# Optimization experiments

Measured on AMD Instinct MI355X. Metric: run time of the kernel, lower is better.

## Reference

```python
import jax, jax.numpy as jnp
import numpy as np

B, L, D = 4096, 200, 128  # batch, neighbor bonds per molecule, bond feature dim
LN_EPS = 1e-5


def setup_inputs() -> dict:
    key = jax.random.key(0)
    ks = jax.random.split(key, 6)
    s = 1.0 / np.sqrt(D).astype(np.float32)
    return {
        "mol_bond_feature": jax.random.normal(ks[0], (B, D), jnp.float32),
        "bond_feature": jax.random.normal(ks[1], (B, L, D), jnp.float32),
        "mol_bond_attend_mask": jnp.ones((B, L, 1), jnp.float32),
        "mol_bond_softmax_mask": jnp.zeros((B, L, 1), jnp.float32),
        "W_self": jax.random.normal(ks[2], (D, D), jnp.float32) * s,   # mol_bond_fc
        "b_self": jnp.zeros((D,), jnp.float32),
        "W_nb": jax.random.normal(ks[3], (D, D), jnp.float32) * s,     # mol_bond_neighbor_fc
        "b_nb": jnp.zeros((D,), jnp.float32),
        "w_align": jax.random.normal(ks[4], (2 * D,), jnp.float32) * s,  # GAT align weight [2D]->1
        "b_align": jnp.zeros((), jnp.float32),
        "ln_gamma": jnp.ones((D,), jnp.float32),
        "ln_beta": jnp.zeros((D,), jnp.float32),
    }


def reference(mol_bond_feature, bond_feature, mol_bond_attend_mask,
              mol_bond_softmax_mask, W_self, b_self, W_nb, b_nb,
              w_align, b_align, ln_gamma, ln_beta):
    # Linear projections (dropout p=0 -> identity)
    x = mol_bond_feature @ W_self.T + b_self            # [B, D]
    y = jnp.einsum('bld,ed->ble', bond_feature, W_nb) + b_nb  # [B, L, D]

    # GAT align: Linear over concat([x_expand, y]) == split dot products (no concat materialized)
    wx, wy = w_align[:D], w_align[D:]
    score = (x @ wx)[:, None, None] + jnp.einsum('bld,d->bl', y, wy)[..., None] + b_align  # [B, L, 1]
    score = jax.nn.leaky_relu(score)                    # GNN_attn_act
    score = score + mol_bond_softmax_mask

    attn = jax.nn.softmax(score, axis=-2) * mol_bond_attend_mask  # [B, L, 1]
    ctx = jnp.sum(attn * y, axis=-2)                    # [B, D]

    # LayerNorm
    mu = jnp.mean(ctx, axis=-1, keepdims=True)
    var = jnp.mean(jnp.square(ctx - mu), axis=-1, keepdims=True)
    return (ctx - mu) * jax.lax.rsqrt(var + LN_EPS) * ln_gamma + ln_beta
```

## Files before the change

### kernel.cpp

```cpp
#include <hip/hip_runtime.h>
#include <math.h>

#define B_ 4096
#define L_ 200
#define D_ 128

typedef float f4 __attribute__((ext_vector_type(4)));

#define WS_AFIN 512
#define WS_WT   5120
#define WS_NEED ((size_t)(WS_WT + D_ * D_) * sizeof(float))

__global__ void prep_kernel(const float* __restrict__ W_self,
                            const float* __restrict__ W_nb,
                            const float* __restrict__ b_self,
                            const float* __restrict__ b_nb,
                            const float* __restrict__ w_align,
                            const float* __restrict__ b_align,
                            float* __restrict__ ws, int do_wt) {
  const int blk = blockIdx.x;
  const int t = threadIdx.x;
  if (blk == 0) {
    float su = 0.f, sv = 0.f;
    for (int e = 0; e < D_; ++e) {
      su = fmaf(w_align[e],      W_self[e * D_ + t], su);
      sv = fmaf(w_align[D_ + e], W_nb[e * D_ + t],   sv);
    }
    ws[t]      = su;
    ws[D_ + t] = sv;
    if (t == 0) {
      float cb = 0.f, cc = 0.f;
      for (int e = 0; e < D_; ++e) {
        cb = fmaf(b_self[e], w_align[e],      cb);
        cc = fmaf(b_nb[e],   w_align[D_ + e], cc);
      }
      ws[2 * D_]     = cb;
      ws[2 * D_ + 1] = cc + b_align[0];
    }
  } else if (do_wt) {
    const int d = blk - 1;
    ws[WS_WT + d * D_ + t] = W_nb[t * D_ + d];
  }
}

template <bool SPLIT>
__global__ __launch_bounds__(256) void mol_bond_stream(
    const float* __restrict__ mbf,
    const float* __restrict__ bond,
    const float* __restrict__ amask,
    const float* __restrict__ smask,
    const float* __restrict__ W_nb,
    const float* __restrict__ b_nb,
    const float* __restrict__ gamma,
    const float* __restrict__ beta,
    float* __restrict__ ws,
    float* __restrict__ out) {
  const int b    = blockIdx.x;
  const int tid  = threadIdx.x;
  const int w    = tid >> 6;
  const int lane = tid & 63;
  const int g    = lane >> 4;
  const int sl   = lane & 15;
  const int dA   = 4 * sl;
  const int dB   = 64 + 4 * sl;
  const int rg   = w * 4 + g;

  __shared__ float am_s[L_];
  __shared__ float sm_s[L_];
  __shared__ float g_l[16][D_];
  __shared__ float sA[16][2];
  __shared__ float gfin[D_];
  __shared__ float ctx_l[D_];
  __shared__ float Afin_s;

  for (int l0 = tid; l0 < L_; l0 += 256) {
    am_s[l0] = amask[(size_t)b * L_ + l0];
    sm_s[l0] = smask[(size_t)b * L_ + l0];
  }

  const f4 uA = *(const f4*)(ws + dA);
  const f4 uB = *(const f4*)(ws + dB);
  const f4 vA = *(const f4*)(ws + D_ + dA);
  const f4 vB = *(const f4*)(ws + D_ + dB);
  const float cb = ws[2 * D_], cc = ws[2 * D_ + 1];

  const f4 mA = *(const f4*)(mbf + (size_t)b * D_ + dA);
  const f4 mB = *(const f4*)(mbf + (size_t)b * D_ + dB);
  float xp = mA.x * uA.x + mA.y * uA.y + mA.z * uA.z + mA.w * uA.w
           + mB.x * uB.x + mB.y * uB.y + mB.z * uB.z + mB.w * uB.w;
  xp += __shfl_xor(xp, 8, 64);
  xp += __shfl_xor(xp, 4, 64);
  xp += __shfl_xor(xp, 2, 64);
  xp += __shfl_xor(xp, 1, 64);
  const float xc = xp + cb + cc;

  __syncthreads();

  float s = 0.f, A = 0.f;
  f4 gA = {0.f, 0.f, 0.f, 0.f};
  f4 gB = {0.f, 0.f, 0.f, 0.f};
  const float* bb = bond + (size_t)b * (L_ * D_);

  auto body = [&](int l) {
    f4 fA = __builtin_nontemporal_load((const f4*)(bb + l * D_ + dA));
    f4 fB = __builtin_nontemporal_load((const f4*)(bb + l * D_ + dB));
    float t = fA.x * vA.x + fA.y * vA.y + fA.z * vA.z + fA.w * vA.w
            + fB.x * vB.x + fB.y * vB.y + fB.z * vB.z + fB.w * vB.w;
    t += __shfl_xor(t, 8, 64);
    t += __shfl_xor(t, 4, 64);
    t += __shfl_xor(t, 2, 64);
    t += __shfl_xor(t, 1, 64);
    float sc = xc + t;
    sc = fmaxf(sc, 0.f) + 0.01f * fminf(sc, 0.f);
    float p  = __expf(sc + sm_s[l]);
    float pa = p * am_s[l];
    s += p;
    A += pa;
    gA.x = fmaf(pa, fA.x, gA.x);
    gA.y = fmaf(pa, fA.y, gA.y);
    gA.z = fmaf(pa, fA.z, gA.z);
    gA.w = fmaf(pa, fA.w, gA.w);
    gB.x = fmaf(pa, fB.x, gB.x);
    gB.y = fmaf(pa, fB.y, gB.y);
    gB.z = fmaf(pa, fB.z, gB.z);
    gB.w = fmaf(pa, fB.w, gB.w);
  };

  int l = rg;
  #pragma unroll 4
  for (int it = 0; it < 12; ++it, l += 16) body(l);
  if (rg < 8) body(192 + rg);

  *(f4*)&g_l[rg][dA] = gA;
  *(f4*)&g_l[rg][dB] = gB;
  if (sl == 0) { sA[rg][0] = s; sA[rg][1] = A; }
  __syncthreads();

  if (tid < D_) {
    float gs = 0.f, st = 0.f, At = 0.f;
    #pragma unroll
    for (int k = 0; k < 16; ++k) {
      gs += g_l[k][tid];
      st += sA[k][0];
      At += sA[k][1];
    }
    float inv = 1.0f / st;
    if constexpr (SPLIT) {
      out[(size_t)b * D_ + tid] = gs * inv;
      if (tid == 0) ws[WS_AFIN + b] = At * inv;
    } else {
      gfin[tid] = gs * inv;
      if (tid == 0) Afin_s = At * inv;
    }
  }

  if constexpr (!SPLIT) {
    __syncthreads();
    if (tid < D_) {
      const int e = tid;
      const f4* Wr = (const f4*)(W_nb + (size_t)e * D_);
      float acc = b_nb[e] * Afin_s;
      #pragma unroll 8
      for (int k = 0; k < D_ / 4; ++k) {
        f4 wv = Wr[k];
        acc += wv.x * gfin[4 * k]     + wv.y * gfin[4 * k + 1]
             + wv.z * gfin[4 * k + 2] + wv.w * gfin[4 * k + 3];
      }
      ctx_l[e] = acc;
    }
    __syncthreads();
    if (tid < 64) {
      float c0 = ctx_l[lane], c1 = ctx_l[lane + 64];
      float t0 = c0 + c1;
      for (int o = 32; o >= 1; o >>= 1) t0 += __shfl_xor(t0, o, 64);
      float mu = t0 * (1.0f / 128.0f);
      float dd0 = c0 - mu, dd1 = c1 - mu;
      float v0 = dd0 * dd0 + dd1 * dd1;
      for (int o = 32; o >= 1; o >>= 1) v0 += __shfl_xor(v0, o, 64);
      float inv = rsqrtf(v0 * (1.0f / 128.0f) + 1e-5f);
      out[(size_t)b * D_ + lane]      = dd0 * inv * gamma[lane]      + beta[lane];
      out[(size_t)b * D_ + lane + 64] = dd1 * inv * gamma[lane + 64] + beta[lane + 64];
    }
  }
}

__global__ __launch_bounds__(256) void ctx_ln_kernel(
    const float* __restrict__ b_nb, const float* __restrict__ gamma,
    const float* __restrict__ beta, const float* __restrict__ ws,
    float* __restrict__ out) {
  const int tid  = threadIdx.x;
  const int slot = tid >> 5;
  const int st   = tid & 31;
  const int b0   = blockIdx.x * 8;
  __shared__ float gq[8][D_];
  __shared__ float Af[8];
  for (int i = tid; i < 8 * D_; i += 256)
    gq[i >> 7][i & 127] = out[(size_t)(b0 + (i >> 7)) * D_ + (i & 127)];
  if (tid < 8) Af[tid] = ws[WS_AFIN + b0 + tid];
  __syncthreads();

  const int b  = b0 + slot;
  const int e0 = 4 * st;
  f4 bn = *(const f4*)(b_nb + e0);
  f4 acc = bn * Af[slot];
  const float* WT = ws + WS_WT;
  #pragma unroll 8
  for (int d = 0; d < D_; ++d) {
    f4 wv = *(const f4*)(WT + d * D_ + e0);
    float gd = gq[slot][d];
    acc.x = fmaf(gd, wv.x, acc.x);
    acc.y = fmaf(gd, wv.y, acc.y);
    acc.z = fmaf(gd, wv.z, acc.z);
    acc.w = fmaf(gd, wv.w, acc.w);
  }
  float sum = acc.x + acc.y + acc.z + acc.w;
  sum += __shfl_xor(sum, 16, 64);
  sum += __shfl_xor(sum, 8, 64);
  sum += __shfl_xor(sum, 4, 64);
  sum += __shfl_xor(sum, 2, 64);
  sum += __shfl_xor(sum, 1, 64);
  float mu = sum * (1.0f / 128.0f);
  f4 dd = acc - mu;
  float vs = dd.x * dd.x + dd.y * dd.y + dd.z * dd.z + dd.w * dd.w;
  vs += __shfl_xor(vs, 16, 64);
  vs += __shfl_xor(vs, 8, 64);
  vs += __shfl_xor(vs, 4, 64);
  vs += __shfl_xor(vs, 2, 64);
  vs += __shfl_xor(vs, 1, 64);
  float inv = rsqrtf(vs * (1.0f / 128.0f) + 1e-5f);
  f4 ga = *(const f4*)(gamma + e0);
  f4 be = *(const f4*)(beta + e0);
  f4 r  = dd * inv * ga + be;
  *(f4*)(out + (size_t)b * D_ + e0) = r;
}

extern "C" void kernel_launch(void* const* d_in, const int* in_sizes, int n_in,
                              void* d_out, int out_size, void* d_ws, size_t ws_size,
                              hipStream_t stream) {
  const float* mbf     = (const float*)d_in[0];
  const float* bond    = (const float*)d_in[1];
  const float* amask   = (const float*)d_in[2];
  const float* smask   = (const float*)d_in[3];
  const float* W_self  = (const float*)d_in[4];
  const float* b_self  = (const float*)d_in[5];
  const float* W_nb    = (const float*)d_in[6];
  const float* b_nb    = (const float*)d_in[7];
  const float* w_align = (const float*)d_in[8];
  const float* b_align = (const float*)d_in[9];
  const float* gamma   = (const float*)d_in[10];
  const float* beta    = (const float*)d_in[11];
  float* ws  = (float*)d_ws;
  float* out = (float*)d_out;

  const bool split = ws_size >= WS_NEED;
  prep_kernel<<<1 + D_, D_, 0, stream>>>(W_self, W_nb, b_self, b_nb, w_align,
                                         b_align, ws, split ? 1 : 0);
  if (split) {
    mol_bond_stream<true><<<B_, 256, 0, stream>>>(mbf, bond, amask, smask, W_nb,
                                                  b_nb, gamma, beta, ws, out);
    ctx_ln_kernel<<<B_ / 8, 256, 0, stream>>>(b_nb, gamma, beta, ws, out);
  } else {
    mol_bond_stream<false><<<B_, 256, 0, stream>>>(mbf, bond, amask, smask, W_nb,
                                                   b_nb, gamma, beta, ws, out);
  }
}
```

Baseline: 89.50 us.

## Register-block ctx_ln GEMM over four molecules per thread and pack mask loads

The ctx+LayerNorm kernel now handles 32 molecules per block, and each thread accumulates four molecules. It reads a transposed, padded shared tile of the gated features, so each loaded weight vector is reused four times and global weight traffic drops. The stream kernel packs the attend and softmax masks into one float2 shared array and raises the loop unroll. The prep kernel parallelises the bias dot products through shared memory. The main risk is fewer blocks for the GEMM kernel (128) and higher register use, while the dominant bandwidth-bound stream kernel barely changes.

```diff
diff --git a/kernel.cpp b/kernel.cpp
--- a/kernel.cpp
+++ b/kernel.cpp
@@ -21,6 +21,7 @@
   const int blk = blockIdx.x;
   const int t = threadIdx.x;
   if (blk == 0) {
+    __shared__ float r1[D_], r2[D_];
     float su = 0.f, sv = 0.f;
     for (int e = 0; e < D_; ++e) {
       su = fmaf(w_align[e],      W_self[e * D_ + t], su);
@@ -28,12 +29,12 @@
     }
     ws[t]      = su;
     ws[D_ + t] = sv;
+    r1[t] = b_self[t] * w_align[t];
+    r2[t] = b_nb[t]   * w_align[D_ + t];
+    __syncthreads();
     if (t == 0) {
       float cb = 0.f, cc = 0.f;
-      for (int e = 0; e < D_; ++e) {
-        cb = fmaf(b_self[e], w_align[e],      cb);
-        cc = fmaf(b_nb[e],   w_align[D_ + e], cc);
-      }
+      for (int e = 0; e < D_; ++e) { cb += r1[e]; cc += r2[e]; }
       ws[2 * D_]     = cb;
       ws[2 * D_ + 1] = cc + b_align[0];
     }
@@ -65,18 +66,15 @@
   const int dB   = 64 + 4 * sl;
   const int rg   = w * 4 + g;
 
-  __shared__ float am_s[L_];
-  __shared__ float sm_s[L_];
+  __shared__ float2 ms[L_];
   __shared__ float g_l[16][D_];
   __shared__ float sA[16][2];
   __shared__ float gfin[D_];
   __shared__ float ctx_l[D_];
   __shared__ float Afin_s;
 
-  for (int l0 = tid; l0 < L_; l0 += 256) {
-    am_s[l0] = amask[(size_t)b * L_ + l0];
-    sm_s[l0] = smask[(size_t)b * L_ + l0];
-  }
+  for (int l0 = tid; l0 < L_; l0 += 256)
+    ms[l0] = make_float2(amask[(size_t)b * L_ + l0], smask[(size_t)b * L_ + l0]);
 
   const f4 uA = *(const f4*)(ws + dA);
   const f4 uB = *(const f4*)(ws + dB);
@@ -112,8 +110,9 @@
     t += __shfl_xor(t, 1, 64);
     float sc = xc + t;
     sc = fmaxf(sc, 0.f) + 0.01f * fminf(sc, 0.f);
-    float p  = __expf(sc + sm_s[l]);
-    float pa = p * am_s[l];
+    float2 m2 = ms[l];
+    float p  = __expf(sc + m2.y);
+    float pa = p * m2.x;
     s += p;
     A += pa;
     gA.x = fmaf(pa, fA.x, gA.x);
@@ -127,7 +126,7 @@
   };
 
   int l = rg;
-  #pragma unroll 4
+  #pragma unroll 6
   for (int it = 0; it < 12; ++it, l += 16) body(l);
   if (rg < 8) body(192 + rg);
 
@@ -191,47 +190,66 @@
   const int tid  = threadIdx.x;
   const int slot = tid >> 5;
   const int st   = tid & 31;
-  const int b0   = blockIdx.x * 8;
-  __shared__ float gq[8][D_];
-  __shared__ float Af[8];
-  for (int i = tid; i < 8 * D_; i += 256)
-    gq[i >> 7][i & 127] = out[(size_t)(b0 + (i >> 7)) * D_ + (i & 127)];
-  if (tid < 8) Af[tid] = ws[WS_AFIN + b0 + tid];
+  const int e0   = 4 * st;
+  const int b0   = blockIdx.x * 32;
+
+  #define GQP 36
+  __shared__ float gqT[D_ * GQP];
+  __shared__ float Af[32];
+
+  for (int i = tid; i < 32 * 32; i += 256) {
+    const int bi = i >> 5;
+    const int d4 = (i & 31) * 4;
+    f4 gv = *(const f4*)(out + (size_t)(b0 + bi) * D_ + d4);
+    gqT[(d4 + 0) * GQP + bi] = gv.x;
+    gqT[(d4 + 1) * GQP + bi] = gv.y;
+    gqT[(d4 + 2) * GQP + bi] = gv.z;
+    gqT[(d4 + 3) * GQP + bi] = gv.w;
+  }
+  if (tid < 32) Af[tid] = ws[WS_AFIN + b0 + tid];
   __syncthreads();
 
-  const int b  = b0 + slot;
-  const int e0 = 4 * st;
-  f4 bn = *(const f4*)(b_nb + e0);
-  f4 acc = bn * Af[slot];
+  const f4 bn = *(const f4*)(b_nb + e0);
+  f4 a0 = bn * Af[slot * 4 + 0];
+  f4 a1 = bn * Af[slot * 4 + 1];
+  f4 a2 = bn * Af[slot * 4 + 2];
+  f4 a3 = bn * Af[slot * 4 + 3];
+
   const float* WT = ws + WS_WT;
-  #pragma unroll 8
+  #pragma unroll 4
   for (int d = 0; d < D_; ++d) {
-    f4 wv = *(const f4*)(WT + d * D_ + e0);
-    float gd = gq[slot][d];
-    acc.x = fmaf(gd, wv.x, acc.x);
-    acc.y = fmaf(gd, wv.y, acc.y);
-    acc.z = fmaf(gd, wv.z, acc.z);
-    acc.w = fmaf(gd, wv.w, acc.w);
-  }
-  float sum = acc.x + acc.y + acc.z + acc.w;
-  sum += __shfl_xor(sum, 16, 64);
-  sum += __shfl_xor(sum, 8, 64);
-  sum += __shfl_xor(sum, 4, 64);
-  sum += __shfl_xor(sum, 2, 64);
-  sum += __shfl_xor(sum, 1, 64);
-  float mu = sum * (1.0f / 128.0f);
-  f4 dd = acc - mu;
-  float vs = dd.x * dd.x + dd.y * dd.y + dd.z * dd.z + dd.w * dd.w;
-  vs += __shfl_xor(vs, 16, 64);
-  vs += __shfl_xor(vs, 8, 64);
-  vs += __shfl_xor(vs, 4, 64);
-  vs += __shfl_xor(vs, 2, 64);
-  vs += __shfl_xor(vs, 1, 64);
-  float inv = rsqrtf(vs * (1.0f / 128.0f) + 1e-5f);
-  f4 ga = *(const f4*)(gamma + e0);
-  f4 be = *(const f4*)(beta + e0);
-  f4 r  = dd * inv * ga + be;
-  *(f4*)(out + (size_t)b * D_ + e0) = r;
+    const f4 wv = *(const f4*)(WT + d * D_ + e0);
+    const f4 g4 = *(const f4*)(&gqT[d * GQP + slot * 4]);
+    a0 += wv * g4.x;
+    a1 += wv * g4.y;
+    a2 += wv * g4.z;
+    a3 += wv * g4.w;
+  }
+
+  const f4 ga = *(const f4*)(gamma + e0);
+  const f4 be = *(const f4*)(beta + e0);
+  f4 accs[4] = {a0, a1, a2, a3};
+  #pragma unroll
+  for (int j = 0; j < 4; ++j) {
+    f4 acc = accs[j];
+    float sum = acc.x + acc.y + acc.z + acc.w;
+    sum += __shfl_xor(sum, 16, 64);
+    sum += __shfl_xor(sum, 8, 64);
+    sum += __shfl_xor(sum, 4, 64);
+    sum += __shfl_xor(sum, 2, 64);
+    sum += __shfl_xor(sum, 1, 64);
+    const float mu = sum * (1.0f / 128.0f);
+    f4 dd = acc - mu;
+    float vs = dd.x * dd.x + dd.y * dd.y + dd.z * dd.z + dd.w * dd.w;
+    vs += __shfl_xor(vs, 16, 64);
+    vs += __shfl_xor(vs, 8, 64);
+    vs += __shfl_xor(vs, 4, 64);
+    vs += __shfl_xor(vs, 2, 64);
+    vs += __shfl_xor(vs, 1, 64);
+    const float inv = rsqrtf(vs * (1.0f / 128.0f) + 1e-5f);
+    const f4 r = dd * inv * ga + be;
+    *(f4*)(out + (size_t)(b0 + slot * 4 + j) * D_ + e0) = r;
+  }
 }
 
 extern "C" void kernel_launch(void* const* d_in, const int* in_sizes, int n_in,
@@ -258,7 +276,7 @@
   if (split) {
     mol_bond_stream<true><<<B_, 256, 0, stream>>>(mbf, bond, amask, smask, W_nb,
                                                   b_nb, gamma, beta, ws, out);
-    ctx_ln_kernel<<<B_ / 8, 256, 0, stream>>>(b_nb, gamma, beta, ws, out);
+    ctx_ln_kernel<<<B_ / 32, 256, 0, stream>>>(b_nb, gamma, beta, ws, out);
   } else {
     mol_bond_stream<false><<<B_, 256, 0, stream>>>(mbf, bond, amask, smask, W_nb,
                                                    b_nb, gamma, beta, ws, out);
```

Measured after the change: 90.53 us. No clear change (+1.1%).
